# Kernel optimization log

Measured on AMD Instinct MI355X. Metric: run time of the kernel, lower is better.

The kernel has to match this reference:

```python
import jax, jax.numpy as jnp
import numpy as np

B, S, H = 2, 2048, 2048
NH = 16
NOPE, ROPE, VDIM, RANK = 128, 64, 128, 512
QHD = NOPE + ROPE  # 192
MAX_POS, THETA = 4096, 50000.0
EPS = 1e-6


def rms_norm(x, w):
    var = jnp.mean(x.astype(jnp.float32) ** 2, axis=-1, keepdims=True)
    return (x * jax.lax.rsqrt(var + EPS)).astype(x.dtype) * w


def deinterleave(x):
    # view(..., d//2, 2).transpose(-1,-2).reshape(..., d): [x0,x2,...,x1,x3,...]
    return jnp.concatenate([x[..., ::2], x[..., 1::2]], axis=-1)


def rotate_half(x):
    x1, x2 = jnp.split(x, 2, axis=-1)
    return jnp.concatenate([-x2, x1], axis=-1)


def setup_inputs() -> dict:
    key = jax.random.key(0)
    ks = jax.random.split(key, 6)
    hidden_states = jax.random.normal(ks[0], (B, S, H), dtype=jnp.float32)
    attention_mask = jnp.broadcast_to(jnp.tril(jnp.ones((S, S), dtype=bool))[None, None], (B, 1, S, S))
    position_ids = jnp.broadcast_to(jnp.arange(S, dtype=jnp.int32)[None], (B, S))
    inv_freq = 1.0 / (THETA ** (jnp.arange(0, ROPE, 2, dtype=jnp.float32) / ROPE))
    freqs = jnp.arange(MAX_POS, dtype=jnp.float32)[:, None] * inv_freq[None, :]
    emb = jnp.concatenate([freqs, freqs], axis=-1)
    cos_cache, sin_cache = jnp.cos(emb), jnp.sin(emb)
    Wq = jax.random.normal(ks[1], (H, NH * QHD), dtype=jnp.float32) * 0.02
    Wkv_a = jax.random.normal(ks[2], (H, RANK + ROPE), dtype=jnp.float32) * 0.02
    kv_a_ln_w = jnp.ones((RANK,), dtype=jnp.float32)
    Wkv_b = jax.random.normal(ks[3], (NH, NOPE + VDIM, RANK), dtype=jnp.float32) * 0.02
    Wo = jax.random.normal(ks[4], (NH * VDIM, H), dtype=jnp.float32) * 0.02
    return {"hidden_states": hidden_states, "attention_mask": attention_mask, "position_ids": position_ids,
            "cos_cache": cos_cache, "sin_cache": sin_cache, "Wq": Wq, "Wkv_a": Wkv_a,
            "kv_a_ln_w": kv_a_ln_w, "Wkv_b": Wkv_b, "Wo": Wo}


def reference(hidden_states, attention_mask, position_ids, cos_cache, sin_cache, Wq, Wkv_a, kv_a_ln_w, Wkv_b, Wo):
    bsz, q_len, _ = hidden_states.shape
    scale = QHD ** (-0.5)
    # Q projection: [b,s,h*192] -> [b,h,s,192]
    q = (hidden_states @ Wq).reshape(bsz, q_len, NH, QHD).transpose(0, 2, 1, 3)
    q_nope, q_pe = q[..., :NOPE], q[..., NOPE:]
    # compressed KV + shared rope key: [b,s,576]
    ckv_full = hidden_states @ Wkv_a
    compressed_kv, k_pe = ckv_full[..., :RANK], ckv_full[..., RANK:]
    compressed_kv = rms_norm(compressed_kv, kv_a_ln_w)  # [b,s,512]
    # interleaved -> half layout, then standard RoPE
    q_pe = deinterleave(q_pe)                     # [b,h,s,64]
    k_pe = deinterleave(k_pe)                     # [b,s,64]
    cos = cos_cache[position_ids][:, None]        # [b,1,s,64]
    sin = sin_cache[position_ids][:, None]
    q_pe = q_pe * cos + rotate_half(q_pe) * sin
    k_pe = (k_pe[:, None] * cos + rotate_half(k_pe[:, None]) * sin)[:, 0]  # [b,s,64]
    # weight absorption
    q_absorb = Wkv_b[:, :NOPE]    # [h,128,512]
    out_absorb = Wkv_b[:, NOPE:]  # [h,128,512]
    q_nope_c = jnp.einsum('hdc,bhqd->bhqc', q_absorb, q_nope)  # [b,h,s,512]
    scores = (jnp.einsum('bhqd,bkd->bhqk', q_pe, k_pe)
              + jnp.einsum('bhqc,bkc->bhqk', q_nope_c, compressed_kv)) * scale
    scores = jnp.where(attention_mask, scores, jnp.float32(-1e9))
    probs = jax.nn.softmax(scores.astype(jnp.float32), axis=-1).astype(hidden_states.dtype)
    x = jnp.einsum('bhqk,bkc->bhqc', probs, compressed_kv)     # [b,h,s,512]
    attn = jnp.einsum('bhqc,hdc->bhqd', x, out_absorb)         # [b,h,s,128]
    attn = attn.transpose(0, 2, 1, 3).reshape(bsz, q_len, NH * VDIM)
    return attn @ Wo
```

## Files before the change

kernel.cpp:

```cpp
#include <hip/hip_runtime.h>
#include <math.h>

#define B_    2
#define S_    2048
#define H_    2048
#define NH_   16
#define NOPE_ 128
#define ROPE_ 64
#define VDIM_ 128
#define RANK_ 512
#define QHD_  192
#define DTOT_ 576

typedef short short8 __attribute__((ext_vector_type(8)));
typedef float f32x4 __attribute__((ext_vector_type(4)));

__device__ __forceinline__ unsigned short f2bf(float f) {
    unsigned u = __float_as_uint(f);
    u += 0x7fffu + ((u >> 16) & 1u);
    return (unsigned short)(u >> 16);
}
__device__ __forceinline__ float bf2f(unsigned short u) {
    return __uint_as_float((unsigned)u << 16);
}
__device__ __forceinline__ unsigned pack2bf(float a, float b) {
    return (unsigned)f2bf(a) | ((unsigned)f2bf(b) << 16);
}
__device__ __forceinline__ unsigned long long pack4bf(float a, float b, float c, float d) {
    return (unsigned long long)pack2bf(a, b) | ((unsigned long long)pack2bf(c, d) << 32);
}
union i4s8 { int4 i; short8 s; };

typedef __attribute__((address_space(3))) unsigned int lds_u32_t;
typedef __attribute__((address_space(1))) const unsigned int glob_u32_t;
__device__ __forceinline__ void async_copy16(const unsigned short* g, unsigned short* l) {
    __builtin_amdgcn_global_load_lds((glob_u32_t*)g, (lds_u32_t*)l, 16, 0, 0);
}

__global__ __launch_bounds__(256) void cast_bf16(const float* __restrict__ in,
                                                 unsigned short* __restrict__ out)
{
    const size_t i = ((size_t)blockIdx.x * 256 + threadIdx.x) * 4;
    float4 v = *(const float4*)(in + i);
    *(unsigned long long*)(out + i) = pack4bf(v.x, v.y, v.z, v.w);
}

__global__ __launch_bounds__(256) void transpose_w(const float* __restrict__ in,
                                                   unsigned short* __restrict__ out,
                                                   int Rr, int Cc,
                                                   size_t inBatch, size_t outBatch)
{
    __shared__ unsigned short tl[64][72];
    in  += (size_t)blockIdx.z * inBatch;
    out += (size_t)blockIdx.z * outBatch;
    const int t  = threadIdx.x;
    const int r0 = blockIdx.x * 64;
    const int c0 = blockIdx.y * 64;
    const int lr = t >> 4;
    const int lc = (t & 15) * 4;
#pragma unroll
    for (int r = 0; r < 4; ++r) {
        float4 v = *(const float4*)(in + (size_t)(r0 + lr*4 + r) * Cc + c0 + lc);
        tl[lr*4 + r][lc+0] = f2bf(v.x); tl[lr*4 + r][lc+1] = f2bf(v.y);
        tl[lr*4 + r][lc+2] = f2bf(v.z); tl[lr*4 + r][lc+3] = f2bf(v.w);
    }
    __syncthreads();
#pragma unroll
    for (int r = 0; r < 4; ++r) {
        ushort4 v;
        v.x = tl[lc+0][lr*4+r]; v.y = tl[lc+1][lr*4+r];
        v.z = tl[lc+2][lr*4+r]; v.w = tl[lc+3][lr*4+r];
        *(ushort4*)(out + (size_t)(c0 + lr*4 + r) * Rr + r0 + lc) = v;
    }
}

#define XCD_SWZ(BX, BY)                                                            \
    {                                                                              \
        const int nx = gridDim.x;                                                  \
        const int nwg = nx * gridDim.y;                                            \
        const int wg = BY * nx + BX;                                               \
        const int nw = (wg & 7) * (nwg >> 3) + (wg >> 3);                          \
        BX = nw % nx; BY = nw / nx;                                                \
    }

#define BGEMM_BODY(STORE_STMT)                                                     \
    __shared__ unsigned short Al[128*32];                                          \
    __shared__ unsigned short Bl[128*32];                                          \
    const int t = threadIdx.x;                                                     \
    const int wv = t >> 6;                                                         \
    const int lane = t & 63;                                                       \
    const int lq = lane & 15, quad = lane >> 4;                                    \
    const int m0 = by * 128, n0 = bx * 128;                                        \
    const int wrow = (wv >> 1) * 64, wcol = (wv & 1) * 64;                         \
    const int srow = lane >> 2;                                                    \
    const int scol = (lane & 3) * 8;                                               \
    f32x4 acc[4][4] = {};                                                          \
    for (int k0 = 0; k0 < K; k0 += 32) {                                           \
        _Pragma("unroll")                                                          \
        for (int pA = 0; pA < 2; ++pA) {                                           \
            const unsigned short* src =                                            \
                A + (size_t)(m0 + pA*64 + wv*16 + srow) * lda + k0 + scol;         \
            async_copy16(src, &Al[pA*2048 + wv*512]);                              \
        }                                                                          \
        _Pragma("unroll")                                                          \
        for (int pB = 0; pB < 2; ++pB) {                                           \
            int brow = n0 + pB*64 + wv*16 + srow;                                  \
            if (brow > N - 1) brow = N - 1;                                        \
            const unsigned short* src = B + (size_t)brow * ldb + k0 + scol;        \
            async_copy16(src, &Bl[pB*2048 + wv*512]);                              \
        }                                                                          \
        __syncthreads();                                                           \
        short8 af[4], bf[4];                                                       \
        _Pragma("unroll")                                                          \
        for (int i = 0; i < 4; ++i) {                                              \
            af[i] = *(const short8*)&Al[(wrow + i*16 + lq)*32 + quad*8];           \
            bf[i] = *(const short8*)&Bl[(wcol + i*16 + lq)*32 + quad*8];           \
        }                                                                          \
        _Pragma("unroll")                                                          \
        for (int mi = 0; mi < 4; ++mi)                                             \
            _Pragma("unroll")                                                      \
            for (int ni = 0; ni < 4; ++ni)                                         \
                acc[mi][ni] = __builtin_amdgcn_mfma_f32_16x16x32_bf16(             \
                    af[mi], bf[ni], acc[mi][ni], 0, 0, 0);                         \
        __syncthreads();                                                           \
    }                                                                              \
    _Pragma("unroll")                                                              \
    for (int mi = 0; mi < 4; ++mi)                                                 \
        _Pragma("unroll")                                                          \
        for (int ni = 0; ni < 4; ++ni) {                                           \
            int col = n0 + wcol + ni*16 + lq;                                      \
            if (col < N) {                                                         \
                _Pragma("unroll")                                                  \
                for (int r = 0; r < 4; ++r)                                        \
                    STORE_STMT;                                                    \
            }                                                                      \
        }

__global__ __launch_bounds__(256, 2) void bgemm2(const unsigned short* __restrict__ A,
                                                 int lda,
                                                 const unsigned short* __restrict__ B,
                                                 int ldb,
                                                 unsigned short* __restrict__ C,
                                                 int ldc, int K, int N, int qcmode)
{
    int bx = blockIdx.x, by = blockIdx.y;
    if (qcmode == 1) {
        const int z = blockIdx.z;
        A += (size_t)(z >> 4) * S_ * (NH_*QHD_) + (z & 15) * QHD_;
        B += (size_t)(z & 15) * RANK_ * NOPE_;
        C += (size_t)z * S_ * DTOT_;
    } else if (qcmode == 2) {
        const int z = blockIdx.z;
        A += (size_t)(z & 15) * 256 * RANK_ + (size_t)NOPE_ * RANK_;
        B += (size_t)(z >> 4) * S_ * DTOT_;
        C += (size_t)z * VDIM_ * S_;
    } else {
        XCD_SWZ(bx, by);
    }
    BGEMM_BODY(C[(size_t)(m0 + wrow + mi*16 + quad*4 + r) * ldc + col] = f2bf(acc[mi][ni][r]))
}

#define PHASE_BAR() { __builtin_amdgcn_sched_barrier(0);                           \
    asm volatile("" ::: "memory");                                                 \
    __builtin_amdgcn_s_barrier();                                                  \
    asm volatile("" ::: "memory");                                                 \
    __builtin_amdgcn_sched_barrier(0); }

#define STG_A(Q, TT) {                                                             \
    const unsigned short* s_ = A + (size_t)(m0 + (Q)*128) * lda + (TT)*64 + stA;   \
    async_copy16(s_,                  &sA[((TT)&1)*16384 + (Q)*8192 + wid*512]);   \
    async_copy16(s_ + (size_t)64*lda, &sA[((TT)&1)*16384 + (Q)*8192 + 4096 + wid*512]); }
#define STG_B(Q, TT) {                                                             \
    const unsigned short* s_ = B + (size_t)(n0 + (Q)*128) * ldb + (TT)*64 + stB;   \
    async_copy16(s_,                  &sB[((TT)&1)*16384 + (Q)*8192 + wid*512]);   \
    async_copy16(s_ + (size_t)64*ldb, &sB[((TT)&1)*16384 + (Q)*8192 + 4096 + wid*512]); }

#define G256_BODY(STORE_STMT)                                                      \
    __shared__ unsigned short sA[2*16384];                                         \
    __shared__ unsigned short sB[2*16384];                                         \
    const int t    = threadIdx.x;                                                  \
    const int wid  = t >> 6;                                                       \
    const int lane = t & 63;                                                       \
    const int lq = lane & 15, quad = lane >> 4;                                    \
    const int wm = wid >> 2, wn = wid & 3;                                         \
    int bx = blockIdx.x, by = blockIdx.y;                                          \
    XCD_SWZ(bx, by);                                                               \
    const int m0 = by * 256, n0 = bx * 256;                                        \
    const int nt = K >> 6;                                                         \
    const int trow = t >> 3;                                                       \
    const int gcol = ((t & 7) ^ (trow & 7)) * 8;                                   \
    const size_t stA = (size_t)trow * lda + gcol;                                  \
    const size_t stB = (size_t)trow * ldb + gcol;                                  \
    const int swz  = lq & 7;                                                       \
    const int selA = (swz >> 2) * 32;                                              \
    const int selB2 = 32 - selA;                                                   \
    const int kqo  = (quad ^ (swz & 3)) * 8;                                       \
    const int aoff = (wm*128 + lq)*64 + kqo;                                       \
    const int boff = (wn*64  + lq)*64 + kqo;                                       \
    f32x4 acc[8][4] = {};                                                          \
                       \
    STG_B(0, 0); STG_A(0, 0); STG_A(1, 0); STG_B(1, 0);                            \
    STG_B(0, 1); STG_A(0, 1);                                                      \
    asm volatile("s_waitcnt vmcnt(4)" ::: "memory");                               \
    PHASE_BAR();                                                                   \
    for (int u = 0; u < nt; ++u) {                                                 \
        const unsigned short* aB = &sA[(u & 1)*16384 + aoff];                      \
        const unsigned short* bB = &sB[(u & 1)*16384 + boff];                      \
        short8 a03[4][2], a47[4][2], b01[2][2], b23[2][2];                         \
                                                                \
        _Pragma("unroll")                                                          \
        for (int rf = 0; rf < 4; ++rf) {                                           \
            a03[rf][0] = *(const short8*)(aB + rf*1024 + selA);                    \
            a03[rf][1] = *(const short8*)(aB + rf*1024 + selB2);                   \
        }                                                                          \
        _Pragma("unroll")                                                          \
        for (int nf = 0; nf < 2; ++nf) {                                           \
            b01[nf][0] = *(const short8*)(bB + nf*1024 + selA);                    \
            b01[nf][1] = *(const short8*)(bB + nf*1024 + selB2);                   \
        }                                                                          \
        if (u + 1 < nt) { STG_A(1, u + 1); }                                       \
        _Pragma("unroll")                                                          \
        for (int rf = 0; rf < 4; ++rf)                                             \
            _Pragma("unroll")                                                      \
            for (int nf = 0; nf < 2; ++nf) {                                       \
                acc[rf][nf] = __builtin_amdgcn_mfma_f32_16x16x32_bf16(             \
                    a03[rf][0], b01[nf][0], acc[rf][nf], 0, 0, 0);                 \
                acc[rf][nf] = __builtin_amdgcn_mfma_f32_16x16x32_bf16(             \
                    a03[rf][1], b01[nf][1], acc[rf][nf], 0, 0, 0);                 \
            }                                                                      \
        PHASE_BAR();                                                               \
                                                                \
        _Pragma("unroll")                                                          \
        for (int nf = 0; nf < 2; ++nf) {                                           \
            b23[nf][0] = *(const short8*)(bB + (2 + nf)*1024 + selA);              \
            b23[nf][1] = *(const short8*)(bB + (2 + nf)*1024 + selB2);             \
        }                                                                          \
        if (u + 1 < nt) { STG_B(1, u + 1); }                                       \
        _Pragma("unroll")                                                          \
        for (int rf = 0; rf < 4; ++rf)                                             \
            _Pragma("unroll")                                                      \
            for (int nf = 0; nf < 2; ++nf) {                                       \
                acc[rf][2 + nf] = __builtin_amdgcn_mfma_f32_16x16x32_bf16(         \
                    a03[rf][0], b23[nf][0], acc[rf][2 + nf], 0, 0, 0);             \
                acc[rf][2 + nf] = __builtin_amdgcn_mfma_f32_16x16x32_bf16(         \
                    a03[rf][1], b23[nf][1], acc[rf][2 + nf], 0, 0, 0);             \
            }                                                                      \
        PHASE_BAR();                                                               \
                                                                \
        _Pragma("unroll")                                                          \
        for (int rf = 0; rf < 4; ++rf) {                                           \
            a47[rf][0] = *(const short8*)(aB + (4 + rf)*1024 + selA);              \
            a47[rf][1] = *(const short8*)(aB + (4 + rf)*1024 + selB2);             \
        }                                                                          \
        if (u + 2 < nt) { STG_B(0, u + 2); }                                       \
        _Pragma("unroll")                                                          \
        for (int rf = 0; rf < 4; ++rf)                                             \
            _Pragma("unroll")                                                      \
            for (int nf = 0; nf < 2; ++nf) {                                       \
                acc[4 + rf][nf] = __builtin_amdgcn_mfma_f32_16x16x32_bf16(         \
                    a47[rf][0], b01[nf][0], acc[4 + rf][nf], 0, 0, 0);             \
                acc[4 + rf][nf] = __builtin_amdgcn_mfma_f32_16x16x32_bf16(         \
                    a47[rf][1], b01[nf][1], acc[4 + rf][nf], 0, 0, 0);             \
            }                                                                      \
        PHASE_BAR();                                                               \
                                                                \
        if (u + 2 < nt) { STG_A(0, u + 2); }                                       \
        _Pragma("unroll")                                                          \
        for (int rf = 0; rf < 4; ++rf)                                             \
            _Pragma("unroll")                                                      \
            for (int nf = 0; nf < 2; ++nf) {                                       \
                acc[4 + rf][2 + nf] = __builtin_amdgcn_mfma_f32_16x16x32_bf16(     \
                    a47[rf][0], b23[nf][0], acc[4 + rf][2 + nf], 0, 0, 0);         \
                acc[4 + rf][2 + nf] = __builtin_amdgcn_mfma_f32_16x16x32_bf16(     \
                    a47[rf][1], b23[nf][1], acc[4 + rf][2 + nf], 0, 0, 0);         \
            }                                                                      \
        if (u + 2 < nt) { asm volatile("s_waitcnt vmcnt(4)" ::: "memory"); }       \
        else            { asm volatile("s_waitcnt vmcnt(0)" ::: "memory"); }       \
        PHASE_BAR();                                                               \
    }                                                                              \
    _Pragma("unroll")                                                              \
    for (int rf = 0; rf < 8; ++rf)                                                 \
        _Pragma("unroll")                                                          \
        for (int nf = 0; nf < 4; ++nf) {                                           \
            const size_t rb = (size_t)(m0 + wm*128 + rf*16 + quad*4) * ldc         \
                              + n0 + wn*64 + nf*16 + lq;                           \
            _Pragma("unroll")                                                      \
            for (int r = 0; r < 4; ++r)                                            \
                STORE_STMT;                                                        \
        }

__global__ __launch_bounds__(512, 2) void gemm256(const unsigned short* __restrict__ A,
                                                  int lda,
                                                  const unsigned short* __restrict__ B,
                                                  int ldb,
                                                  unsigned short* __restrict__ C,
                                                  int ldc, int K)
{
    G256_BODY(C[rb + (size_t)r*ldc] = f2bf(acc[rf][nf][r]))
}

__global__ __launch_bounds__(512, 2) void gemm256f(const unsigned short* __restrict__ A,
                                                   int lda,
                                                   const unsigned short* __restrict__ B,
                                                   int ldb,
                                                   float* __restrict__ C,
                                                   int ldc, int K)
{
    G256_BODY(C[rb + (size_t)r*ldc] = acc[rf][nf][r])
}

__global__ __launch_bounds__(128) void postkv(const unsigned short* __restrict__ ckv_bf,
                                              const float* __restrict__ lnw,
                                              const int*   __restrict__ pos_ids,
                                              const float* __restrict__ cosc,
                                              const float* __restrict__ sinc,
                                              unsigned short* __restrict__ k_cat)
{
    const int row = blockIdx.x;
    const int t   = threadIdx.x;
    const unsigned short* src = ckv_bf + (size_t)row * DTOT_;
    __shared__ float red[128];

    ushort4 v = *(const ushort4*)(src + t * 4);
    float x0 = bf2f(v.x), x1 = bf2f(v.y), x2 = bf2f(v.z), x3 = bf2f(v.w);
    red[t] = x0*x0 + x1*x1 + x2*x2 + x3*x3;
    __syncthreads();
    for (int off = 64; off > 0; off >>= 1) {
        if (t < off) red[t] += red[t + off];
        __syncthreads();
    }
    const float rs = rsqrtf(red[0] / (float)RANK_ + 1e-6f);

    unsigned short* kc = k_cat + (size_t)row * DTOT_;
    *(unsigned long long*)(kc + t*4) =
        pack4bf(x0*rs*lnw[t*4+0], x1*rs*lnw[t*4+1], x2*rs*lnw[t*4+2], x3*rs*lnw[t*4+3]);

    if (t < 32) {
        const int pos = pos_ids[row];
        const float c  = cosc[pos * ROPE_ + t];
        const float sn = sinc[pos * ROPE_ + t];
        const float y0 = bf2f(src[RANK_ + 2*t]);
        const float y1 = bf2f(src[RANK_ + 2*t + 1]);
        kc[RANK_ + t]      = f2bf(y0*c - y1*sn);
        kc[RANK_ + 32 + t] = f2bf(y1*c + y0*sn);
    }
}

__global__ __launch_bounds__(512) void ropeq(const unsigned short* __restrict__ q_bf,
                                             const int*   __restrict__ pos_ids,
                                             const float* __restrict__ cosc,
                                             const float* __restrict__ sinc,
                                             unsigned short* __restrict__ q_cat)
{
    const int row = blockIdx.x;
    const int t   = threadIdx.x;
    const int h   = t >> 5;
    const int i   = t & 31;
    const int pos = pos_ids[row];
    const float c  = cosc[pos * ROPE_ + i];
    const float sn = sinc[pos * ROPE_ + i];
    const unsigned short* qrow = q_bf + (size_t)row * (NH_*QHD_) + h * QHD_ + NOPE_;
    const float x0 = bf2f(qrow[2*i]);
    const float x1 = bf2f(qrow[2*i + 1]);
    const int b = row >> 11, s = row & 2047;
    unsigned short* qc = q_cat + ((size_t)(b * NH_ + h) * S_ + s) * DTOT_ + RANK_;
    qc[i]      = f2bf(x0*c - x1*sn);
    qc[32 + i] = f2bf(x1*c + x0*sn);
}

__global__ __launch_bounds__(256) void wcast(const float* __restrict__ w,
                                             unsigned short* __restrict__ wbf)
{
    const size_t i = ((size_t)blockIdx.x * 256 + threadIdx.x) * 4;
    float4 v = *(const float4*)(w + i);
    *(unsigned long long*)(wbf + i) = pack4bf(v.x, v.y, v.z, v.w);
}

__device__ __forceinline__ short8 quad_transpose(unsigned d0, unsigned d1,
                                                 unsigned d2, unsigned d3,
                                                 int srcA, int srcB, bool lowquad)
{
    int e0 = __shfl((int)d0, srcA, 64);
    int e1 = __shfl((int)d1, srcA, 64);
    int e2 = __shfl((int)d2, srcA, 64);
    int e3 = __shfl((int)d3, srcA, 64);
    int f0 = __shfl((int)d0, srcB, 64);
    int f1 = __shfl((int)d1, srcB, 64);
    int f2 = __shfl((int)d2, srcB, 64);
    int f3 = __shfl((int)d3, srcB, 64);
    i4s8 u;
    u.i.x = lowquad ? e0 : e2;
    u.i.y = lowquad ? e1 : e3;
    u.i.z = lowquad ? f0 : f2;
    u.i.w = lowquad ? f1 : f3;
    return u.s;
}

__global__ __launch_bounds__(256, 2) void flash_attn4(
    const unsigned short* __restrict__ q_cat,
    const unsigned short* __restrict__ k_cat,
    const unsigned short* __restrict__ vwt,
    unsigned short* __restrict__ attn_bf)
{
    __shared__ unsigned short sKa[32*512];
    __shared__ unsigned short sKb[32*64];
    __shared__ unsigned short sVW[128*32];

    const int t    = threadIdx.x;
    const int wv   = t >> 6;
    const int lane = t & 63;
    const int lq   = lane & 15;
    const int quad = lane >> 4;
    const int h    = blockIdx.x;
    const int q0   = (31 - blockIdx.y) * 64;
    const int b    = blockIdx.z;
    const int srcA = lq + ((quad & 1) << 5);
    const int srcB = srcA + 16;
    const bool lowq = quad < 2;
    const int myq  = q0 + wv*16 + lq;

    const unsigned short* qrow =
        q_cat + (((size_t)(b*NH_ + h)) * S_ + q0 + wv*16 + lq) * DTOT_ + quad*8;
    short8 qf[18];
#pragma unroll
    for (int c = 0; c < 18; ++c) qf[c] = *(const short8*)(qrow + c*32);

    const unsigned short* kcb = k_cat + (size_t)b * S_ * DTOT_;
    const unsigned short* vtb = vwt + (size_t)(b*NH_ + h) * VDIM_ * S_;

    f32x4 o[8];
#pragma unroll
    for (int i = 0; i < 8; ++i) o[i] = (f32x4){0.f, 0.f, 0.f, 0.f};
    float m_i = -1e30f, l_i = 0.f;
    const float scale = 0.0721687836f;
    const int ntiles = (q0 >> 5) + 2;

    const int swz  = lq & 7;
    const int selA = (swz >> 2) * 32;
    const int selB = 32 - selA;
    const int kqo  = (quad ^ (swz & 3)) * 8;
    const unsigned short* kr0a = &sKa[lq*512 + kqo];
    const unsigned short* kr1a = &sKa[(16 + lq)*512 + kqo];
    const unsigned short* kr0b = &sKb[lq*64 + kqo];
    const unsigned short* kr1b = &sKb[(16 + lq)*64 + kqo];

    const int kq0 = wv*DTOT_ + (lane ^ wv)*8;
    const int kq1 = wv*DTOT_ + (lane ^ (wv + 4))*8;
    const int kob = (t >> 3)*DTOT_ + RANK_ + ((t & 7) ^ ((t >> 3) & 7))*8;

    const int vrow  = wv*16 + (lane >> 2);
    const int vgcol = (((lane & 3) ^ ((lane >> 3) & 3))) * 8;
    const int pvsw  = (quad ^ ((lq >> 1) & 3)) * 8;

#define ISSUE_K(TPTR)                                                          \
    _Pragma("unroll")                                                          \
    for (int p = 0; p < 8; ++p)                                                \
        async_copy16((TPTR) + (p*4)*DTOT_ + ((p & 1) ? kq1 : kq0),             \
                     &sKa[p*2048 + wv*512]);                                   \
    async_copy16((TPTR) + kob, &sKb[wv*512])

    const unsigned short* ktp = kcb;
    ISSUE_K(ktp);
    ktp += 32 * DTOT_;

    for (int tt = 0; tt < ntiles; ++tt) {
        const int k0 = tt << 5;
        __syncthreads();
        {
#pragma unroll
            for (int p = 0; p < 2; ++p) {
                const unsigned short* vsrc =
                    vtb + (size_t)(p*64 + vrow) * S_ + k0 + vgcol;
                async_copy16(vsrc, &sVW[p*2048 + wv*512]);
            }
        }
        f32x4 s0a = {0.f,0.f,0.f,0.f}, s0b = {0.f,0.f,0.f,0.f};
        f32x4 s1a = {0.f,0.f,0.f,0.f}, s1b = {0.f,0.f,0.f,0.f};
#pragma unroll
        for (int c = 0; c < 16; c += 2) {
            short8 ka0 = *(const short8*)(kr0a + c*32 + selA);
            short8 kb0 = *(const short8*)(kr0a + c*32 + selB);
            short8 ka1 = *(const short8*)(kr1a + c*32 + selA);
            short8 kb1 = *(const short8*)(kr1a + c*32 + selB);
            s0a = __builtin_amdgcn_mfma_f32_16x16x32_bf16(ka0, qf[c],   s0a, 0, 0, 0);
            s1a = __builtin_amdgcn_mfma_f32_16x16x32_bf16(ka1, qf[c],   s1a, 0, 0, 0);
            s0b = __builtin_amdgcn_mfma_f32_16x16x32_bf16(kb0, qf[c+1], s0b, 0, 0, 0);
            s1b = __builtin_amdgcn_mfma_f32_16x16x32_bf16(kb1, qf[c+1], s1b, 0, 0, 0);
        }
        {
            short8 ka0 = *(const short8*)(kr0b + selA);
            short8 kb0 = *(const short8*)(kr0b + selB);
            short8 ka1 = *(const short8*)(kr1b + selA);
            short8 kb1 = *(const short8*)(kr1b + selB);
            s0a = __builtin_amdgcn_mfma_f32_16x16x32_bf16(ka0, qf[16], s0a, 0, 0, 0);
            s1a = __builtin_amdgcn_mfma_f32_16x16x32_bf16(ka1, qf[16], s1a, 0, 0, 0);
            s0b = __builtin_amdgcn_mfma_f32_16x16x32_bf16(kb0, qf[17], s0b, 0, 0, 0);
            s1b = __builtin_amdgcn_mfma_f32_16x16x32_bf16(kb1, qf[17], s1b, 0, 0, 0);
        }
        float sv[8];
#pragma unroll
        for (int r = 0; r < 4; ++r) {
            int kk0 = k0 + quad*4 + r;
            sv[r]     = (kk0      <= myq) ? (s0a[r] + s0b[r]) * scale : -1e30f;
            sv[r + 4] = (kk0 + 16 <= myq) ? (s1a[r] + s1b[r]) * scale : -1e30f;
        }
        float mx = sv[0];
#pragma unroll
        for (int i = 1; i < 8; ++i) mx = fmaxf(mx, sv[i]);
        mx = fmaxf(mx, __shfl_xor(mx, 16));
        mx = fmaxf(mx, __shfl_xor(mx, 32));
        if (!__all(mx <= m_i + 8.f)) {
            const float m_new = fmaxf(m_i, mx);
            const float alpha = __expf(m_i - m_new);
            m_i = m_new;
            l_i *= alpha;
#pragma unroll
            for (int i = 0; i < 8; ++i) {
                o[i][0]*=alpha; o[i][1]*=alpha; o[i][2]*=alpha; o[i][3]*=alpha;
            }
        }
        float p[8]; float ls = 0.f;
#pragma unroll
        for (int i = 0; i < 8; ++i) { p[i] = __expf(sv[i] - m_i); ls += p[i]; }
        ls += __shfl_xor(ls, 16);
        ls += __shfl_xor(ls, 32);
        l_i += ls;
        short8 pb = quad_transpose(pack2bf(p[0], p[1]), pack2bf(p[2], p[3]),
                                   pack2bf(p[4], p[5]), pack2bf(p[6], p[7]),
                                   srcA, srcB, lowq);
        __syncthreads();
        if (tt + 1 < ntiles) {
            ISSUE_K(ktp);
            ktp += 32 * DTOT_;
        }
#pragma unroll
        for (int dt = 0; dt < 8; ++dt) {
            short8 va = *(const short8*)&sVW[(dt*16 + lq)*32 + pvsw];
            o[dt] = __builtin_amdgcn_mfma_f32_16x16x32_bf16(va, pb, o[dt], 0, 0, 0);
        }
    }

    const float inv = 1.0f / l_i;
    unsigned short* orow =
        attn_bf + ((size_t)b * S_ + q0 + wv*16 + lq) * (NH_*VDIM_) + h*VDIM_;
#pragma unroll
    for (int dt2 = 0; dt2 < 4; ++dt2) {
        short8 xa = quad_transpose(
            pack2bf(o[2*dt2][0]*inv,   o[2*dt2][1]*inv),
            pack2bf(o[2*dt2][2]*inv,   o[2*dt2][3]*inv),
            pack2bf(o[2*dt2+1][0]*inv, o[2*dt2+1][1]*inv),
            pack2bf(o[2*dt2+1][2]*inv, o[2*dt2+1][3]*inv),
            srcA, srcB, lowq);
        *(short8*)(orow + dt2*32 + quad*8) = xa;
    }
}

extern "C" void kernel_launch(void* const* d_in, const int* in_sizes, int n_in,
                              void* d_out, int out_size, void* d_ws, size_t ws_size,
                              hipStream_t stream)
{
    const float* hidden  = (const float*)d_in[0];
    const int*   pos_ids = (const int*)d_in[2];
    const float* cosc    = (const float*)d_in[3];
    const float* sinc    = (const float*)d_in[4];
    const float* Wq      = (const float*)d_in[5];
    const float* Wkv_a   = (const float*)d_in[6];
    const float* lnw     = (const float*)d_in[7];
    const float* Wkv_b   = (const float*)d_in[8];
    const float* Wo      = (const float*)d_in[9];
    float* out = (float*)d_out;

    const int M = B_ * S_;
    char* ws = (char*)d_ws;
    unsigned short* hidden_bf = (unsigned short*)ws;
    unsigned short* vwT       = (unsigned short*)ws;
    unsigned short* q_bf      = (unsigned short*)(ws + 16777216);
    unsigned short* attn_bf   = q_bf;
    unsigned short* ckv_bf    = (unsigned short*)(ws + 41943040);
    unsigned short* wqaT      = ckv_bf;
    unsigned short* q_cat     = (unsigned short*)(ws + 46661632);
    unsigned short* k_cat     = (unsigned short*)(ws + 122159104);
    unsigned short* wT        = (unsigned short*)(ws + 126877696);
    unsigned short* w2bf      = (unsigned short*)(ws + 126877696 + 8388608);

    cast_bf16<<<8192, 256, 0, stream>>>(hidden, hidden_bf);
    transpose_w<<<dim3(32, 48, 1), 256, 0, stream>>>(Wq, wT, H_, NH_*QHD_, 0, 0);
    gemm256<<<dim3(12, 16), 512, 0, stream>>>(hidden_bf, H_, wT, H_, q_bf, NH_*QHD_, H_);
    transpose_w<<<dim3(32, 9, 1), 256, 0, stream>>>(Wkv_a, wT, H_, DTOT_, 0, 0);
    bgemm2<<<dim3(5, 32, 1), 256, 0, stream>>>(hidden_bf, H_, wT, H_, ckv_bf, DTOT_, H_, DTOT_, 0);
    postkv<<<M, 128, 0, stream>>>(ckv_bf, lnw, pos_ids, cosc, sinc, k_cat);
    ropeq<<<M, 512, 0, stream>>>(q_bf, pos_ids, cosc, sinc, q_cat);
    wcast<<<(NH_*256*RANK_)/1024, 256, 0, stream>>>(Wkv_b, w2bf);
    bgemm2<<<dim3(16, 1, 32), 256, 0, stream>>>(w2bf, RANK_, k_cat, DTOT_, vwT, S_, RANK_, S_, 2);
    transpose_w<<<dim3(2, 8, 16), 256, 0, stream>>>(Wkv_b, wqaT, NOPE_, RANK_,
                                                    (size_t)256*RANK_, (size_t)RANK_*NOPE_);
    bgemm2<<<dim3(4, 16, 32), 256, 0, stream>>>(q_bf, NH_*QHD_, wqaT, NOPE_, q_cat, DTOT_, NOPE_, RANK_, 1);
    flash_attn4<<<dim3(NH_, S_/64, B_), 256, 0, stream>>>(q_cat, k_cat, vwT, attn_bf);
    transpose_w<<<dim3(32, 32, 1), 256, 0, stream>>>(Wo, wT, H_, H_, 0, 0);
    gemm256f<<<dim3(8, 16), 512, 0, stream>>>(attn_bf, H_, wT, H_, out, H_, H_);
}
```

Measured before the change: 518.9 us.

## Add MFMA priority hints and use 256x128 tiles for output projection GEMM

Wraps the MFMA blocks in the 256x256 GEMM with s_setprio(1)/s_setprio(0) so waves issuing matrix math get scheduling priority over waves issuing loads. Replaces the output-projection GEMM (256x256 tiles, 128 blocks) with a new 256x128-tile kernel launched on 256 blocks, which gives the 256-CU device more blocks to fill it. The trade-off is less data reuse per tile and a new pipeline schedule with a different vmcnt wait depth.

Result: no change. 509.5 us (-1.8%).

```diff
diff --git a/kernel.cpp b/kernel.cpp
--- a/kernel.cpp
+++ b/kernel.cpp
@@ -219,6 +219,7 @@
             b01[nf][1] = *(const short8*)(bB + nf*1024 + selB2);                   \
         }                                                                          \
         if (u + 1 < nt) { STG_A(1, u + 1); }                                       \
+        __builtin_amdgcn_s_setprio(1);                                             \
         _Pragma("unroll")                                                          \
         for (int rf = 0; rf < 4; ++rf)                                             \
             _Pragma("unroll")                                                      \
@@ -228,6 +229,7 @@
                 acc[rf][nf] = __builtin_amdgcn_mfma_f32_16x16x32_bf16(             \
                     a03[rf][1], b01[nf][1], acc[rf][nf], 0, 0, 0);                 \
             }                                                                      \
+        __builtin_amdgcn_s_setprio(0);                                             \
         PHASE_BAR();                                                               \
                                                                 \
         _Pragma("unroll")                                                          \
@@ -236,6 +238,7 @@
             b23[nf][1] = *(const short8*)(bB + (2 + nf)*1024 + selB2);             \
         }                                                                          \
         if (u + 1 < nt) { STG_B(1, u + 1); }                                       \
+        __builtin_amdgcn_s_setprio(1);                                             \
         _Pragma("unroll")                                                          \
         for (int rf = 0; rf < 4; ++rf)                                             \
             _Pragma("unroll")                                                      \
@@ -245,6 +248,7 @@
                 acc[rf][2 + nf] = __builtin_amdgcn_mfma_f32_16x16x32_bf16(         \
                     a03[rf][1], b23[nf][1], acc[rf][2 + nf], 0, 0, 0);             \
             }                                                                      \
+        __builtin_amdgcn_s_setprio(0);                                             \
         PHASE_BAR();                                                               \
                                                                 \
         _Pragma("unroll")                                                          \
@@ -253,6 +257,7 @@
             a47[rf][1] = *(const short8*)(aB + (4 + rf)*1024 + selB2);             \
         }                                                                          \
         if (u + 2 < nt) { STG_B(0, u + 2); }                                       \
+        __builtin_amdgcn_s_setprio(1);                                             \
         _Pragma("unroll")                                                          \
         for (int rf = 0; rf < 4; ++rf)                                             \
             _Pragma("unroll")                                                      \
@@ -262,9 +267,11 @@
                 acc[4 + rf][nf] = __builtin_amdgcn_mfma_f32_16x16x32_bf16(         \
                     a47[rf][1], b01[nf][1], acc[4 + rf][nf], 0, 0, 0);             \
             }                                                                      \
+        __builtin_amdgcn_s_setprio(0);                                             \
         PHASE_BAR();                                                               \
                                                                 \
         if (u + 2 < nt) { STG_A(0, u + 2); }                                       \
+        __builtin_amdgcn_s_setprio(1);                                             \
         _Pragma("unroll")                                                          \
         for (int rf = 0; rf < 4; ++rf)                                             \
             _Pragma("unroll")                                                      \
@@ -274,6 +281,7 @@
                 acc[4 + rf][2 + nf] = __builtin_amdgcn_mfma_f32_16x16x32_bf16(     \
                     a47[rf][1], b23[nf][1], acc[4 + rf][2 + nf], 0, 0, 0);         \
             }                                                                      \
+        __builtin_amdgcn_s_setprio(0);                                             \
         if (u + 2 < nt) { asm volatile("s_waitcnt vmcnt(4)" ::: "memory"); }       \
         else            { asm volatile("s_waitcnt vmcnt(0)" ::: "memory"); }       \
         PHASE_BAR();                                                               \
@@ -299,14 +307,136 @@
     G256_BODY(C[rb + (size_t)r*ldc] = f2bf(acc[rf][nf][r]))
 }
 
-__global__ __launch_bounds__(512, 2) void gemm256f(const unsigned short* __restrict__ A,
-                                                   int lda,
-                                                   const unsigned short* __restrict__ B,
-                                                   int ldb,
-                                                   float* __restrict__ C,
-                                                   int ldc, int K)
-{
-    G256_BODY(C[rb + (size_t)r*ldc] = acc[rf][nf][r])
+__global__ __launch_bounds__(512, 2) void g256x128f(const unsigned short* __restrict__ A,
+                                                    int lda,
+                                                    const unsigned short* __restrict__ B,
+                                                    int ldb,
+                                                    float* __restrict__ C,
+                                                    int ldc, int K)
+{
+    __shared__ unsigned short sA[2*16384];
+    __shared__ unsigned short sB[2*8192];
+    const int t    = threadIdx.x;
+    const int wid  = t >> 6;
+    const int lane = t & 63;
+    const int lq = lane & 15, quad = lane >> 4;
+    const int wm = wid >> 1, wn = wid & 1;
+    int bx = blockIdx.x, by = blockIdx.y;
+    XCD_SWZ(bx, by);
+    const int m0 = by * 256, n0 = bx * 128;
+    const int nt = K >> 6;
+    const int trow = t >> 3;
+    const int gcol = ((t & 7) ^ (trow & 7)) * 8;
+    const size_t stA = (size_t)trow * lda + gcol;
+    const size_t stB = (size_t)trow * ldb + gcol;
+    const int swz  = lq & 7;
+    const int selA = (swz >> 2) * 32;
+    const int selB2 = 32 - selA;
+    const int kqo  = (quad ^ (swz & 3)) * 8;
+    const int aoff = (wm*64 + lq)*64 + kqo;
+    const int boff = (wn*64 + lq)*64 + kqo;
+    f32x4 acc[4][4] = {};
+
+#define STGX_A(Q, TT) {                                                            \
+    const unsigned short* s_ = A + (size_t)(m0 + (Q)*128) * lda + (TT)*64 + stA;   \
+    async_copy16(s_,                  &sA[((TT)&1)*16384 + (Q)*8192 + wid*512]);   \
+    async_copy16(s_ + (size_t)64*lda, &sA[((TT)&1)*16384 + (Q)*8192 + 4096 + wid*512]); }
+#define STGX_B(TT) {                                                               \
+    const unsigned short* s_ = B + (size_t)n0 * ldb + (TT)*64 + stB;               \
+    async_copy16(s_,                  &sB[((TT)&1)*8192 + wid*512]);               \
+    async_copy16(s_ + (size_t)64*ldb, &sB[((TT)&1)*8192 + 4096 + wid*512]); }
+
+    STGX_B(0); STGX_A(0, 0); STGX_A(1, 0);
+    STGX_B(1); STGX_A(0, 1); STGX_A(1, 1);
+    asm volatile("s_waitcnt vmcnt(6)" ::: "memory");
+    PHASE_BAR();
+    for (int u = 0; u < nt; ++u) {
+        const unsigned short* aB = &sA[(u & 1)*16384 + aoff];
+        const unsigned short* bB = &sB[(u & 1)*8192 + boff];
+        short8 a01[2][2], a23[2][2], b01[2][2], b23[2][2];
+#pragma unroll
+        for (int rf = 0; rf < 2; ++rf) {
+            a01[rf][0] = *(const short8*)(aB + rf*1024 + selA);
+            a01[rf][1] = *(const short8*)(aB + rf*1024 + selB2);
+        }
+#pragma unroll
+        for (int nf = 0; nf < 2; ++nf) {
+            b01[nf][0] = *(const short8*)(bB + nf*1024 + selA);
+            b01[nf][1] = *(const short8*)(bB + nf*1024 + selB2);
+        }
+        __builtin_amdgcn_s_setprio(1);
+#pragma unroll
+        for (int rf = 0; rf < 2; ++rf)
+#pragma unroll
+            for (int nf = 0; nf < 2; ++nf) {
+                acc[rf][nf] = __builtin_amdgcn_mfma_f32_16x16x32_bf16(
+                    a01[rf][0], b01[nf][0], acc[rf][nf], 0, 0, 0);
+                acc[rf][nf] = __builtin_amdgcn_mfma_f32_16x16x32_bf16(
+                    a01[rf][1], b01[nf][1], acc[rf][nf], 0, 0, 0);
+            }
+        __builtin_amdgcn_s_setprio(0);
+        PHASE_BAR();
+#pragma unroll
+        for (int nf = 0; nf < 2; ++nf) {
+            b23[nf][0] = *(const short8*)(bB + (2 + nf)*1024 + selA);
+            b23[nf][1] = *(const short8*)(bB + (2 + nf)*1024 + selB2);
+        }
+        __builtin_amdgcn_s_setprio(1);
+#pragma unroll
+        for (int rf = 0; rf < 2; ++rf)
+#pragma unroll
+            for (int nf = 0; nf < 2; ++nf) {
+                acc[rf][2 + nf] = __builtin_amdgcn_mfma_f32_16x16x32_bf16(
+                    a01[rf][0], b23[nf][0], acc[rf][2 + nf], 0, 0, 0);
+                acc[rf][2 + nf] = __builtin_amdgcn_mfma_f32_16x16x32_bf16(
+                    a01[rf][1], b23[nf][1], acc[rf][2 + nf], 0, 0, 0);
+            }
+        __builtin_amdgcn_s_setprio(0);
+        PHASE_BAR();
+#pragma unroll
+        for (int rf = 0; rf < 2; ++rf) {
+            a23[rf][0] = *(const short8*)(aB + (2 + rf)*1024 + selA);
+            a23[rf][1] = *(const short8*)(aB + (2 + rf)*1024 + selB2);
+        }
+        if (u + 2 < nt) { STGX_B(u + 2); }
+        __builtin_amdgcn_s_setprio(1);
+#pragma unroll
+        for (int rf = 0; rf < 2; ++rf)
+#pragma unroll
+            for (int nf = 0; nf < 2; ++nf) {
+                acc[2 + rf][nf] = __builtin_amdgcn_mfma_f32_16x16x32_bf16(
+                    a23[rf][0], b01[nf][0], acc[2 + rf][nf], 0, 0, 0);
+                acc[2 + rf][nf] = __builtin_amdgcn_mfma_f32_16x16x32_bf16(
+                    a23[rf][1], b01[nf][1], acc[2 + rf][nf], 0, 0, 0);
+            }
+        __builtin_amdgcn_s_setprio(0);
+        PHASE_BAR();
+        if (u + 2 < nt) { STGX_A(0, u + 2); STGX_A(1, u + 2); }
+        __builtin_amdgcn_s_setprio(1);
+#pragma unroll
+        for (int rf = 0; rf < 2; ++rf)
+#pragma unroll
+            for (int nf = 0; nf < 2; ++nf) {
+                acc[2 + rf][2 + nf] = __builtin_amdgcn_mfma_f32_16x16x32_bf16(
+                    a23[rf][0], b23[nf][0], acc[2 + rf][2 + nf], 0, 0, 0);
+                acc[2 + rf][2 + nf] = __builtin_amdgcn_mfma_f32_16x16x32_bf16(
+                    a23[rf][1], b23[nf][1], acc[2 + rf][2 + nf], 0, 0, 0);
+            }
+        __builtin_amdgcn_s_setprio(0);
+        if (u + 2 < nt) { asm volatile("s_waitcnt vmcnt(6)" ::: "memory"); }
+        else            { asm volatile("s_waitcnt vmcnt(0)" ::: "memory"); }
+        PHASE_BAR();
+    }
+#pragma unroll
+    for (int rf = 0; rf < 4; ++rf)
+#pragma unroll
+        for (int nf = 0; nf < 4; ++nf) {
+            const size_t rb = (size_t)(m0 + wm*64 + rf*16 + quad*4) * ldc
+                              + n0 + wn*64 + nf*16 + lq;
+#pragma unroll
+            for (int r = 0; r < 4; ++r)
+                C[rb + (size_t)r*ldc] = acc[rf][nf][r];
+        }
 }
 
 __global__ __launch_bounds__(128) void postkv(const unsigned short* __restrict__ ckv_bf,
@@ -597,5 +727,5 @@
     bgemm2<<<dim3(4, 16, 32), 256, 0, stream>>>(q_bf, NH_*QHD_, wqaT, NOPE_, q_cat, DTOT_, NOPE_, RANK_, 1);
     flash_attn4<<<dim3(NH_, S_/64, B_), 256, 0, stream>>>(q_cat, k_cat, vwT, attn_bf);
     transpose_w<<<dim3(32, 32, 1), 256, 0, stream>>>(Wo, wT, H_, H_, 0, 0);
-    gemm256f<<<dim3(8, 16), 512, 0, stream>>>(attn_bf, H_, wT, H_, out, H_, H_);
-}
+    g256x128f<<<dim3(16, 16), 512, 0, stream>>>(attn_bf, H_, wT, H_, out, H_, H_);
+}
```
